# Performance work log

Hardware: AMD Instinct MI355X
Metric: run time of the kernel (lower is better)

Reference implementation:

```python
import jax, jax.numpy as jnp
import numpy as np

# levels for the auction iterations: j = 7..-1 gives level = -4^j, j = -2 gives level = 0
_LEVEL_JS = list(range(7, -3, -1))


def approx_match(xyz1, xyz2):
    # xyz1: [B,N,3], xyz2: [B,M,3] -> soft match matrix [B,N,M]
    B, N, _ = xyz1.shape
    M = xyz2.shape[1]
    multiL = 1.0 if N >= M else float(M // N)
    multiR = float(N // M) if N >= M else 1.0
    # pairwise squared distances [B,N,M]
    d2 = jnp.sum((xyz1[:, :, None, :] - xyz2[:, None, :, :]) ** 2, axis=-1)
    levels = jnp.array([0.0 if j == -2 else -(4.0 ** j) for j in _LEVEL_JS],
                       dtype=xyz1.dtype)

    def step(carry, level):
        match, remainL, remainR = carry
        w = jnp.exp(level * d2) * remainR[:, None, :]                      # [B,N,M]
        # row-normalize to each left point's remaining mass
        w = w * (remainL / (jnp.sum(w, axis=2) + 1e-9))[:, :, None]
        # clip columns to right points' remaining capacity
        ss = jnp.sum(w, axis=1) + 1e-9                                     # [B,M]
        w = w * jnp.minimum(remainR / ss, 1.0)[:, None, :]
        match = match + w
        remainL = jnp.maximum(remainL - jnp.sum(w, axis=2), 0.0)
        remainR = jnp.maximum(remainR - jnp.sum(w, axis=1), 0.0)
        return (match, remainL, remainR), None

    init = (jnp.zeros_like(d2),
            jnp.full((B, N), multiL, dtype=d2.dtype),
            jnp.full((B, M), multiR, dtype=d2.dtype))
    (match, _, _), _ = jax.lax.scan(step, init, levels)
    return match


def match_cost(xyz1, xyz2, match):
    # cost[b] = sum_{k,l} match[b,k,l] * ||xyz1[b,k] - xyz2[b,l]||
    d = jnp.sqrt(jnp.sum((xyz1[:, :, None, :] - xyz2[:, None, :, :]) ** 2, axis=-1))
    return jnp.sum(match * d, axis=(1, 2))


def setup_inputs() -> dict:
    key = jax.random.key(0)
    k1, k2 = jax.random.split(key)
    B, N, M = 8, 2048, 2048
    input1 = jax.random.normal(k1, (B, N, 3), dtype=jnp.float32)
    input2 = jax.random.normal(k2, (B, M, 3), dtype=jnp.float32)
    return {"input1": input1, "input2": input2}


def reference(input1, input2):
    match = approx_match(input1, input2)
    return match_cost(input1, input2, match)
```

## Files before the change

kernel.cpp:

```cpp
#include <hip/hip_runtime.h>
#include <hip/hip_fp16.h>


#define BATCH 8
#define NPTS 2048
#define MPTS 2048
#define BLOCK 256
#define ROWS 16
#define LOG2E 1.44269504088896340736f

__device__ __forceinline__ float fast_exp2(float x) {
  return __builtin_amdgcn_exp2f(x);
}
__device__ __forceinline__ float fast_sqrt(float a) {
  return __builtin_amdgcn_sqrtf(a);
}
__device__ __forceinline__ float packh2(float c, float r) {
  __half2 h = __halves2half2(__float2half_rn(c), __float2half_rn(r));
  return __builtin_bit_cast(float, h);
}

__device__ __forceinline__ void load8(const float4* q, int r0, float k,
                                      float* x, float* y, float* z) {
  int b4 = (r0 >> 2) * 3;
  float4 q0 = q[b4], q1 = q[b4 + 1], q2 = q[b4 + 2];
  float4 q3 = q[b4 + 3], q4 = q[b4 + 4], q5 = q[b4 + 5];
  x[0] = k * q0.x; y[0] = k * q0.y; z[0] = k * q0.z;
  x[1] = k * q0.w; y[1] = k * q1.x; z[1] = k * q1.y;
  x[2] = k * q1.z; y[2] = k * q1.w; z[2] = k * q2.x;
  x[3] = k * q2.y; y[3] = k * q2.z; z[3] = k * q2.w;
  x[4] = k * q3.x; y[4] = k * q3.y; z[4] = k * q3.z;
  x[5] = k * q3.w; y[5] = k * q4.x; z[5] = k * q4.y;
  x[6] = k * q4.z; y[6] = k * q4.w; z[6] = k * q5.x;
  x[7] = k * q5.y; y[7] = k * q5.z; z[7] = k * q5.w;
}

__global__ __launch_bounds__(BLOCK, 4) void emd_A0_kernel(
    const float* __restrict__ xyz1, const float* __restrict__ xyz2,
    float* __restrict__ rowscale, float* __restrict__ out,
    float* __restrict__ t9, float* __restrict__ t1acc,
    float* __restrict__ t1zero, float k0) {
  __shared__ float4 sP[MPTS];
  __shared__ float sRed[ROWS * 4];
  __shared__ float sRs[ROWS];

  const int tid = threadIdx.x;
  const int bid = blockIdx.x;
  const int b = bid >> 7;
  const int t0 = (bid & 127) * ROWS;
  const bool desig = (bid & 127) == 0;
  if (bid == 0 && tid < BATCH) { out[tid] = 0.0f; t9[tid] = 0.0f; }

  const float4* q2 = (const float4*)(xyz2 + (size_t)b * MPTS * 3);
  float4* z4 = (float4*)(t1zero + (size_t)b * MPTS);
  for (int g = tid; g < MPTS / 4; g += BLOCK) {
    float4 a = q2[3 * g], bb = q2[3 * g + 1], c = q2[3 * g + 2];
    sP[4 * g + 0] = make_float4(k0 * a.x, k0 * a.y, k0 * a.z, 0.0f);
    sP[4 * g + 1] = make_float4(k0 * a.w, k0 * bb.x, k0 * bb.y, 0.0f);
    sP[4 * g + 2] = make_float4(k0 * bb.z, k0 * bb.w, k0 * c.x, 0.0f);
    sP[4 * g + 3] = make_float4(k0 * c.y, k0 * c.z, k0 * c.w, 0.0f);
    if (desig) z4[g] = make_float4(0.f, 0.f, 0.f, 0.f);
  }
  __syncthreads();

  const int wave = tid >> 6, lane = tid & 63;
  const int phase = lane >> 1, rg = lane & 1;
  const int r0 = t0 + rg * 8;
  float x1[8], y1[8], z1[8], acc[8];
  load8((const float4*)(xyz1 + (size_t)b * NPTS * 3), r0, k0, x1, y1, z1);
#pragma unroll
  for (int j = 0; j < 8; ++j) acc[j] = 0.0f;
  const int mb = wave * 512 + phase;
#pragma unroll 2
  for (int it = 0; it < 16; ++it) {
    float4 v = sP[mb + it * 32];
#pragma unroll
    for (int j = 0; j < 8; ++j) {
      float dx = x1[j] - v.x, dy = y1[j] - v.y, dz = z1[j] - v.z;
      float s = __builtin_fmaf(dx, dx, __builtin_fmaf(dy, dy, dz * dz));
      acc[j] += fast_exp2(-s);
    }
  }
#pragma unroll
  for (int j = 0; j < 8; ++j) {
    acc[j] += __shfl_xor(acc[j], 2, 64);
    acc[j] += __shfl_xor(acc[j], 4, 64);
    acc[j] += __shfl_xor(acc[j], 8, 64);
    acc[j] += __shfl_xor(acc[j], 16, 64);
    acc[j] += __shfl_xor(acc[j], 32, 64);
  }
  if (lane < 2) {
#pragma unroll
    for (int j = 0; j < 8; ++j) sRed[(rg * 8 + j) * 4 + wave] = acc[j];
  }
  __syncthreads();
  if (tid < ROWS) {
    float s = sRed[tid * 4] + sRed[tid * 4 + 1] + sRed[tid * 4 + 2] +
              sRed[tid * 4 + 3];
    float rs = 1.0f / (s + 1e-9f);
    rowscale[(size_t)b * NPTS + t0 + tid] = rs;
    sRs[tid] = rs;
  }
  __syncthreads();

  float rsn[8];
#pragma unroll
  for (int j = 0; j < 8; ++j) rsn[j] = sRs[rg * 8 + j];
  float* accb = t1acc + (size_t)b * MPTS;
#pragma unroll 2
  for (int it = 0; it < 16; ++it) {
    int idx = mb + it * 32;
    float4 v = sP[idx];
    float part = 0.0f;
#pragma unroll
    for (int j = 0; j < 8; ++j) {
      float dx = x1[j] - v.x, dy = y1[j] - v.y, dz = z1[j] - v.z;
      float s = __builtin_fmaf(dx, dx, __builtin_fmaf(dy, dy, dz * dz));
      part = __builtin_fmaf(fast_exp2(-s), rsn[j], part);
    }
    part += __shfl_xor(part, 1, 64);
    if (rg == 0) atomicAdd(accb + idx, part);
  }
}

template <bool FIRST, bool LAST>
__global__ __launch_bounds__(BLOCK, 4) void emd_CA_kernel(
    const float* __restrict__ xyz1, const float* __restrict__ xyz2,
    float* __restrict__ rowscale, float* __restrict__ remainL,
    const float* __restrict__ rrIn, float* __restrict__ rrOut,
    const float* __restrict__ t1In, float* __restrict__ t1Acc,
    float* __restrict__ t1Zero, float* __restrict__ out,
    float* __restrict__ t9, float kS, float invK) {
  __shared__ float4 sP[MPTS];
  __shared__ float sRedS[ROWS * 4];
  __shared__ float sRedC[ROWS * 4];
  __shared__ float sRedR[ROWS * 4];
  __shared__ float sCost[ROWS];
  __shared__ float sRs[ROWS];

  const int tid = threadIdx.x;
  const int bid = blockIdx.x;
  const int b = bid >> 7;
  const int t0 = (bid & 127) * ROWS;
  const bool desig = (bid & 127) == 0;

  const float4* q2 = (const float4*)(xyz2 + (size_t)b * MPTS * 3);
  const float4* rr4 = (const float4*)(rrIn + (size_t)b * MPTS);
  const float4* t14 = (const float4*)(t1In + (size_t)b * MPTS);
  float4* ro4 = (float4*)(rrOut + (size_t)b * MPTS);
  float4* z4 = LAST ? nullptr : (float4*)(t1Zero + (size_t)b * MPTS);
  for (int g = tid; g < MPTS / 4; g += BLOCK) {
    float4 a = q2[3 * g], bb = q2[3 * g + 1], c = q2[3 * g + 2];
    float4 t1v = t14[g];
    float4 rrv = FIRST ? make_float4(1.f, 1.f, 1.f, 1.f) : rr4[g];
    float cc[4], rn[4];
    float rrc[4] = {rrv.x, rrv.y, rrv.z, rrv.w};
    float t1c[4] = {t1v.x, t1v.y, t1v.z, t1v.w};
#pragma unroll
    for (int i = 0; i < 4; ++i) {
      float colsum = rrc[i] * t1c[i];
      float cs = fminf(rrc[i] / (colsum + 1e-9f), 1.0f);
      cc[i] = rrc[i] * cs;
      rn[i] = fmaxf(rrc[i] - colsum * cs, 0.0f);
    }
    sP[4 * g + 0] = make_float4(kS * a.x, kS * a.y, kS * a.z, packh2(cc[0], rn[0]));
    sP[4 * g + 1] = make_float4(kS * a.w, kS * bb.x, kS * bb.y, packh2(cc[1], rn[1]));
    sP[4 * g + 2] = make_float4(kS * bb.z, kS * bb.w, kS * c.x, packh2(cc[2], rn[2]));
    sP[4 * g + 3] = make_float4(kS * c.y, kS * c.z, kS * c.w, packh2(cc[3], rn[3]));
    if (desig) {
      ro4[g] = make_float4(rn[0], rn[1], rn[2], rn[3]);
      if (!LAST) z4[g] = make_float4(0.f, 0.f, 0.f, 0.f);
    }
  }
  __syncthreads();

  const int wave = tid >> 6, lane = tid & 63;
  const int phase = lane >> 2, rg = lane & 3;
  const int r0 = t0 + rg * 4;
  float x1[4], y1[4], z1[4];
  {
    const float4* q1 = (const float4*)(xyz1 + (size_t)b * NPTS * 3);
    int b4 = (r0 >> 2) * 3;
    float4 a = q1[b4], bb = q1[b4 + 1], c = q1[b4 + 2];
    x1[0] = kS * a.x;  y1[0] = kS * a.y;  z1[0] = kS * a.z;
    x1[1] = kS * a.w;  y1[1] = kS * bb.x; z1[1] = kS * bb.y;
    x1[2] = kS * bb.z; y1[2] = kS * bb.w; z1[2] = kS * c.x;
    x1[3] = kS * c.y;  y1[3] = kS * c.z;  z1[3] = kS * c.w;
  }
  float accS[4] = {0.f, 0.f, 0.f, 0.f};
  float accC[4] = {0.f, 0.f, 0.f, 0.f};
  float accR[4] = {0.f, 0.f, 0.f, 0.f};
  const int mb = wave * 512 + phase;
#pragma unroll 4
  for (int it = 0; it < 32; ++it) {
    float4 v = sP[mb + it * 16];
    __half2 h = __builtin_bit_cast(__half2, v.w);
    float cc = __low2float(h);
    float rr = __high2float(h);
#pragma unroll
    for (int j = 0; j < 4; ++j) {
      float dx = x1[j] - v.x, dy = y1[j] - v.y, dz = z1[j] - v.z;
      float s = __builtin_fmaf(dx, dx, __builtin_fmaf(dy, dy, dz * dz));
      float sq = fast_sqrt(s);
      float e1, e2;
      if (LAST) {
        e2 = 1.0f;
        e1 = fast_exp2(-s);
      } else {
        e2 = fast_exp2(-s);
        float e2s = e2 * e2;
        e1 = e2s * e2s;
      }
      float t = e1 * cc;
      accS[j] += t;
      accC[j] = __builtin_fmaf(t, sq, accC[j]);
      if (LAST) accR[j] += rr;
      else      accR[j] = __builtin_fmaf(e2, rr, accR[j]);
    }
  }
#pragma unroll
  for (int j = 0; j < 4; ++j) {
    accS[j] += __shfl_xor(accS[j], 4, 64);
    accS[j] += __shfl_xor(accS[j], 8, 64);
    accS[j] += __shfl_xor(accS[j], 16, 64);
    accS[j] += __shfl_xor(accS[j], 32, 64);
    accC[j] += __shfl_xor(accC[j], 4, 64);
    accC[j] += __shfl_xor(accC[j], 8, 64);
    accC[j] += __shfl_xor(accC[j], 16, 64);
    accC[j] += __shfl_xor(accC[j], 32, 64);
    accR[j] += __shfl_xor(accR[j], 4, 64);
    accR[j] += __shfl_xor(accR[j], 8, 64);
    accR[j] += __shfl_xor(accR[j], 16, 64);
    accR[j] += __shfl_xor(accR[j], 32, 64);
  }
  if (lane < 4) {
#pragma unroll
    for (int j = 0; j < 4; ++j) {
      sRedS[(rg * 4 + j) * 4 + wave] = accS[j];
      sRedC[(rg * 4 + j) * 4 + wave] = accC[j];
      sRedR[(rg * 4 + j) * 4 + wave] = accR[j];
    }
  }
  __syncthreads();
  if (tid < ROWS) {
    float S2 = sRedS[tid * 4] + sRedS[tid * 4 + 1] + sRedS[tid * 4 + 2] +
               sRedS[tid * 4 + 3];
    float C = sRedC[tid * 4] + sRedC[tid * 4 + 1] + sRedC[tid * 4 + 2] +
              sRedC[tid * 4 + 3];
    float R = sRedR[tid * 4] + sRedR[tid * 4 + 1] + sRedR[tid * 4 + 2] +
              sRedR[tid * 4 + 3];
    size_t idx = (size_t)b * NPTS + t0 + tid;
    float rs = rowscale[idx];
    float rl = FIRST ? 1.0f : remainL[idx];
    float rlN = fmaxf(rl - rs * S2, 0.0f);
    remainL[idx] = rlN;
    float rsN = rlN / (R + 1e-9f);
    rowscale[idx] = rsN;
    sCost[tid] = rs * C * invK;
    sRs[tid] = rsN;
  }
  __syncthreads();
  if (tid == 0) {
    float t = 0.0f;
#pragma unroll
    for (int i = 0; i < ROWS; ++i) t += sCost[i];
    atomicAdd(out + b, t);
    if (LAST) {
      float r = 0.0f;
#pragma unroll
      for (int i = 0; i < ROWS; ++i) r += sRs[i];
      atomicAdd(t9 + b, r);
    }
  }
  if (!LAST) {
    float rsn[4];
#pragma unroll
    for (int j = 0; j < 4; ++j) rsn[j] = sRs[rg * 4 + j];
    float* accb = t1Acc + (size_t)b * MPTS;
#pragma unroll 4
    for (int it = 0; it < 32; ++it) {
      int idx = mb + it * 16;
      float4 v = sP[idx];
      float part = 0.0f;
#pragma unroll
      for (int j = 0; j < 4; ++j) {
        float dx = x1[j] - v.x, dy = y1[j] - v.y, dz = z1[j] - v.z;
        float s = __builtin_fmaf(dx, dx, __builtin_fmaf(dy, dy, dz * dz));
        part = __builtin_fmaf(fast_exp2(-s), rsn[j], part);
      }
      part += __shfl_xor(part, 1, 64);
      part += __shfl_xor(part, 2, 64);
      if (rg == 0) atomicAdd(accb + idx, part);
    }
  }
}

__global__ __launch_bounds__(BLOCK, 4) void emd_C9_kernel(
    const float* __restrict__ xyz1, const float* __restrict__ xyz2,
    const float* __restrict__ rowscale, const float* __restrict__ remainR,
    const float* __restrict__ t9, float* __restrict__ out) {
  __shared__ float4 sP[MPTS];
  __shared__ float sRed[ROWS * 4];
  __shared__ float sCost[ROWS];

  const int tid = threadIdx.x;
  const int bid = blockIdx.x;
  const int b = bid >> 7;
  const int t0 = (bid & 127) * ROWS;
  const int wave = tid >> 6, lane = tid & 63;
  const float t1 = t9[b];

  const float4* q2 = (const float4*)(xyz2 + (size_t)b * MPTS * 3);
  const float4* rr4 = (const float4*)(remainR + (size_t)b * MPTS);
  for (int g = tid; g < MPTS / 4; g += BLOCK) {
    float4 a = q2[3 * g], bb = q2[3 * g + 1], c = q2[3 * g + 2];
    float4 rr = rr4[g];
    float w0 = rr.x * fminf(rr.x / (rr.x * t1 + 1e-9f), 1.0f);
    float w1 = rr.y * fminf(rr.y / (rr.y * t1 + 1e-9f), 1.0f);
    float w2 = rr.z * fminf(rr.z / (rr.z * t1 + 1e-9f), 1.0f);
    float w3 = rr.w * fminf(rr.w / (rr.w * t1 + 1e-9f), 1.0f);
    sP[4 * g + 0] = make_float4(a.x, a.y, a.z, w0);
    sP[4 * g + 1] = make_float4(a.w, bb.x, bb.y, w1);
    sP[4 * g + 2] = make_float4(bb.z, bb.w, c.x, w2);
    sP[4 * g + 3] = make_float4(c.y, c.z, c.w, w3);
  }
  __syncthreads();

  const int phase = lane >> 1, rg = lane & 1;
  const int r0 = t0 + rg * 8;
  float x1[8], y1[8], z1[8], acc[8];
  load8((const float4*)(xyz1 + (size_t)b * NPTS * 3), r0, 1.0f, x1, y1, z1);
#pragma unroll
  for (int j = 0; j < 8; ++j) acc[j] = 0.0f;
  const int mb = wave * 512 + phase;
#pragma unroll 2
  for (int it = 0; it < 16; ++it) {
    float4 v = sP[mb + it * 32];
#pragma unroll
    for (int j = 0; j < 8; ++j) {
      float dx = x1[j] - v.x, dy = y1[j] - v.y, dz = z1[j] - v.z;
      float d2 = __builtin_fmaf(dx, dx, __builtin_fmaf(dy, dy, dz * dz));
      acc[j] = __builtin_fmaf(fast_sqrt(d2), v.w, acc[j]);
    }
  }
#pragma unroll
  for (int j = 0; j < 8; ++j) {
    acc[j] += __shfl_xor(acc[j], 2, 64);
    acc[j] += __shfl_xor(acc[j], 4, 64);
    acc[j] += __shfl_xor(acc[j], 8, 64);
    acc[j] += __shfl_xor(acc[j], 16, 64);
    acc[j] += __shfl_xor(acc[j], 32, 64);
  }
  if (lane < 2) {
#pragma unroll
    for (int j = 0; j < 8; ++j) sRed[(rg * 8 + j) * 4 + wave] = acc[j];
  }
  __syncthreads();
  if (tid < ROWS) {
    float C = sRed[tid * 4] + sRed[tid * 4 + 1] + sRed[tid * 4 + 2] +
              sRed[tid * 4 + 3];
    sCost[tid] = rowscale[(size_t)b * NPTS + t0 + tid] * C;
  }
  __syncthreads();
  if (tid == 0) {
    float t = 0.0f;
#pragma unroll
    for (int i = 0; i < ROWS; ++i) t += sCost[i];
    atomicAdd(out + b, t);
  }
}

extern "C" void kernel_launch(void* const* d_in, const int* in_sizes, int n_in,
                              void* d_out, int out_size, void* d_ws, size_t ws_size,
                              hipStream_t stream) {
  const float* xyz1 = (const float*)d_in[0];
  const float* xyz2 = (const float*)d_in[1];
  float* out = (float*)d_out;
  float* ws = (float*)d_ws;

  const int BN = BATCH * NPTS, BM = BATCH * MPTS;
  float* remainL  = ws;
  float* rowscale = ws + BN;
  float* rrA      = ws + 2 * BN;
  float* rrB      = ws + 2 * BN + BM;
  float* t1b      = ws + 2 * BN + 2 * BM;
  float* t9       = ws + 2 * BN + 5 * BM;

  const float levels[9] = {-16384.f, -4096.f, -1024.f, -256.f, -64.f,
                           -16.f,    -4.f,    -1.f,    -0.25f};
  dim3 grid(BATCH * (NPTS / ROWS));

  hipMemsetAsync(t1b, 0, (size_t)BM * sizeof(float), stream);

  emd_A0_kernel<<<grid, BLOCK, 0, stream>>>(
      xyz1, xyz2, rowscale, out, t9, t1b , t1b + BM ,
      sqrtf(-levels[0] * LOG2E));

  for (int l = 0; l < 9; ++l) {
    float kB = sqrtf(-levels[l] * LOG2E);
    float kA = 0.5f * kB;
    float* cur = t1b + (size_t)(l % 3) * BM;
    float* nxt = t1b + (size_t)((l + 1) % 3) * BM;
    float* zer = t1b + (size_t)((l + 2) % 3) * BM;
    float* rin = (l % 2 == 0) ? rrA : rrB;
    float* rou = (l % 2 == 0) ? rrB : rrA;
    if (l == 0) {
      emd_CA_kernel<true, false><<<grid, BLOCK, 0, stream>>>(
          xyz1, xyz2, rowscale, remainL, rin, rou, cur, nxt, zer, out, t9,
          kA, 1.0f / kA);
    } else if (l < 8) {
      emd_CA_kernel<false, false><<<grid, BLOCK, 0, stream>>>(
          xyz1, xyz2, rowscale, remainL, rin, rou, cur, nxt, zer, out, t9,
          kA, 1.0f / kA);
    } else {
      emd_CA_kernel<false, true><<<grid, BLOCK, 0, stream>>>(
          xyz1, xyz2, rowscale, remainL, rin, rou, cur, nxt, zer, out, t9,
          kB, 1.0f / kB);
    }
  }
  emd_C9_kernel<<<grid, BLOCK, 0, stream>>>(xyz1, xyz2, rowscale, rrB, t9, out);
}
```

Measured before the change: 357.4 us.

## Halve rows per block and stage xyz2 through LDS in two chunks

```diff
diff --git a/kernel.cpp b/kernel.cpp
--- a/kernel.cpp
+++ b/kernel.cpp
@@ -6,7 +6,8 @@
 #define NPTS 2048
 #define MPTS 2048
 #define BLOCK 256
-#define ROWS 16
+#define ROWS 8
+#define CHUNK 1024
 #define LOG2E 1.44269504088896340736f
 
 __device__ __forceinline__ float fast_exp2(float x) {
@@ -35,63 +36,77 @@
   x[7] = k * q5.y; y[7] = k * q5.z; z[7] = k * q5.w;
 }
 
-__global__ __launch_bounds__(BLOCK, 4) void emd_A0_kernel(
+__device__ __forceinline__ void load4(const float4* q, int r0, float k,
+                                      float* x, float* y, float* z) {
+  int b4 = (r0 >> 2) * 3;
+  float4 a = q[b4], bb = q[b4 + 1], c = q[b4 + 2];
+  x[0] = k * a.x;  y[0] = k * a.y;  z[0] = k * a.z;
+  x[1] = k * a.w;  y[1] = k * bb.x; z[1] = k * bb.y;
+  x[2] = k * bb.z; y[2] = k * bb.w; z[2] = k * c.x;
+  x[3] = k * c.y;  y[3] = k * c.z;  z[3] = k * c.w;
+}
+
+__global__ __launch_bounds__(BLOCK, 6) void emd_A0_kernel(
     const float* __restrict__ xyz1, const float* __restrict__ xyz2,
     float* __restrict__ rowscale, float* __restrict__ out,
     float* __restrict__ t9, float* __restrict__ t1acc,
     float* __restrict__ t1zero, float k0) {
-  __shared__ float4 sP[MPTS];
+  __shared__ float4 sP[CHUNK];
   __shared__ float sRed[ROWS * 4];
   __shared__ float sRs[ROWS];
 
   const int tid = threadIdx.x;
   const int bid = blockIdx.x;
-  const int b = bid >> 7;
-  const int t0 = (bid & 127) * ROWS;
-  const bool desig = (bid & 127) == 0;
+  const int b = bid >> 8;
+  const int t0 = (bid & 255) * ROWS;
+  const bool desig = (bid & 255) == 0;
   if (bid == 0 && tid < BATCH) { out[tid] = 0.0f; t9[tid] = 0.0f; }
 
+  const int wave = tid >> 6, lane = tid & 63;
   const float4* q2 = (const float4*)(xyz2 + (size_t)b * MPTS * 3);
   float4* z4 = (float4*)(t1zero + (size_t)b * MPTS);
-  for (int g = tid; g < MPTS / 4; g += BLOCK) {
-    float4 a = q2[3 * g], bb = q2[3 * g + 1], c = q2[3 * g + 2];
-    sP[4 * g + 0] = make_float4(k0 * a.x, k0 * a.y, k0 * a.z, 0.0f);
-    sP[4 * g + 1] = make_float4(k0 * a.w, k0 * bb.x, k0 * bb.y, 0.0f);
-    sP[4 * g + 2] = make_float4(k0 * bb.z, k0 * bb.w, k0 * c.x, 0.0f);
-    sP[4 * g + 3] = make_float4(k0 * c.y, k0 * c.z, k0 * c.w, 0.0f);
-    if (desig) z4[g] = make_float4(0.f, 0.f, 0.f, 0.f);
-  }
-  __syncthreads();
-
-  const int wave = tid >> 6, lane = tid & 63;
-  const int phase = lane >> 1, rg = lane & 1;
-  const int r0 = t0 + rg * 8;
+
   float x1[8], y1[8], z1[8], acc[8];
-  load8((const float4*)(xyz1 + (size_t)b * NPTS * 3), r0, k0, x1, y1, z1);
+  load8((const float4*)(xyz1 + (size_t)b * NPTS * 3), t0, k0, x1, y1, z1);
 #pragma unroll
   for (int j = 0; j < 8; ++j) acc[j] = 0.0f;
-  const int mb = wave * 512 + phase;
-#pragma unroll 2
-  for (int it = 0; it < 16; ++it) {
-    float4 v = sP[mb + it * 32];
-#pragma unroll
-    for (int j = 0; j < 8; ++j) {
-      float dx = x1[j] - v.x, dy = y1[j] - v.y, dz = z1[j] - v.z;
-      float s = __builtin_fmaf(dx, dx, __builtin_fmaf(dy, dy, dz * dz));
-      acc[j] += fast_exp2(-s);
+
+  for (int ch = 0; ch < 2; ++ch) {
+    __syncthreads();
+    {
+      const float4* qc = q2 + ch * (CHUNK * 3 / 4);
+      int g = tid;
+      float4 a = qc[3 * g], bb = qc[3 * g + 1], c = qc[3 * g + 2];
+      sP[4 * g + 0] = make_float4(k0 * a.x, k0 * a.y, k0 * a.z, 0.0f);
+      sP[4 * g + 1] = make_float4(k0 * a.w, k0 * bb.x, k0 * bb.y, 0.0f);
+      sP[4 * g + 2] = make_float4(k0 * bb.z, k0 * bb.w, k0 * c.x, 0.0f);
+      sP[4 * g + 3] = make_float4(k0 * c.y, k0 * c.z, k0 * c.w, 0.0f);
+      if (desig) z4[ch * 256 + g] = make_float4(0.f, 0.f, 0.f, 0.f);
+    }
+    __syncthreads();
+#pragma unroll
+    for (int it = 0; it < 4; ++it) {
+      float4 v = sP[wave * 256 + lane + it * 64];
+#pragma unroll
+      for (int j = 0; j < 8; ++j) {
+        float dx = x1[j] - v.x, dy = y1[j] - v.y, dz = z1[j] - v.z;
+        float s = __builtin_fmaf(dx, dx, __builtin_fmaf(dy, dy, dz * dz));
+        acc[j] += fast_exp2(-s);
+      }
     }
   }
 #pragma unroll
   for (int j = 0; j < 8; ++j) {
+    acc[j] += __shfl_xor(acc[j], 1, 64);
     acc[j] += __shfl_xor(acc[j], 2, 64);
     acc[j] += __shfl_xor(acc[j], 4, 64);
     acc[j] += __shfl_xor(acc[j], 8, 64);
     acc[j] += __shfl_xor(acc[j], 16, 64);
     acc[j] += __shfl_xor(acc[j], 32, 64);
   }
-  if (lane < 2) {
-#pragma unroll
-    for (int j = 0; j < 8; ++j) sRed[(rg * 8 + j) * 4 + wave] = acc[j];
+  if (lane == 0) {
+#pragma unroll
+    for (int j = 0; j < 8; ++j) sRed[j * 4 + wave] = acc[j];
   }
   __syncthreads();
   if (tid < ROWS) {
@@ -105,33 +120,45 @@
 
   float rsn[8];
 #pragma unroll
-  for (int j = 0; j < 8; ++j) rsn[j] = sRs[rg * 8 + j];
+  for (int j = 0; j < 8; ++j) rsn[j] = sRs[j];
   float* accb = t1acc + (size_t)b * MPTS;
-#pragma unroll 2
-  for (int it = 0; it < 16; ++it) {
-    int idx = mb + it * 32;
-    float4 v = sP[idx];
-    float part = 0.0f;
-#pragma unroll
-    for (int j = 0; j < 8; ++j) {
-      float dx = x1[j] - v.x, dy = y1[j] - v.y, dz = z1[j] - v.z;
-      float s = __builtin_fmaf(dx, dx, __builtin_fmaf(dy, dy, dz * dz));
-      part = __builtin_fmaf(fast_exp2(-s), rsn[j], part);
-    }
-    part += __shfl_xor(part, 1, 64);
-    if (rg == 0) atomicAdd(accb + idx, part);
+  for (int ch = 0; ch < 2; ++ch) {
+    __syncthreads();
+    {
+      const float4* qc = q2 + ch * (CHUNK * 3 / 4);
+      int g = tid;
+      float4 a = qc[3 * g], bb = qc[3 * g + 1], c = qc[3 * g + 2];
+      sP[4 * g + 0] = make_float4(k0 * a.x, k0 * a.y, k0 * a.z, 0.0f);
+      sP[4 * g + 1] = make_float4(k0 * a.w, k0 * bb.x, k0 * bb.y, 0.0f);
+      sP[4 * g + 2] = make_float4(k0 * bb.z, k0 * bb.w, k0 * c.x, 0.0f);
+      sP[4 * g + 3] = make_float4(k0 * c.y, k0 * c.z, k0 * c.w, 0.0f);
+    }
+    __syncthreads();
+#pragma unroll
+    for (int it = 0; it < 4; ++it) {
+      int idx = wave * 256 + lane + it * 64;
+      float4 v = sP[idx];
+      float part = 0.0f;
+#pragma unroll
+      for (int j = 0; j < 8; ++j) {
+        float dx = x1[j] - v.x, dy = y1[j] - v.y, dz = z1[j] - v.z;
+        float s = __builtin_fmaf(dx, dx, __builtin_fmaf(dy, dy, dz * dz));
+        part = __builtin_fmaf(fast_exp2(-s), rsn[j], part);
+      }
+      atomicAdd(accb + ch * CHUNK + idx, part);
+    }
   }
 }
 
 template <bool FIRST, bool LAST>
-__global__ __launch_bounds__(BLOCK, 4) void emd_CA_kernel(
+__global__ __launch_bounds__(BLOCK, 6) void emd_CA_kernel(
     const float* __restrict__ xyz1, const float* __restrict__ xyz2,
     float* __restrict__ rowscale, float* __restrict__ remainL,
     const float* __restrict__ rrIn, float* __restrict__ rrOut,
     const float* __restrict__ t1In, float* __restrict__ t1Acc,
     float* __restrict__ t1Zero, float* __restrict__ out,
     float* __restrict__ t9, float kS, float invK) {
-  __shared__ float4 sP[MPTS];
+  __shared__ float4 sP[CHUNK];
   __shared__ float sRedS[ROWS * 4];
   __shared__ float sRedC[ROWS * 4];
   __shared__ float sRedR[ROWS * 4];
@@ -140,100 +167,100 @@
 
   const int tid = threadIdx.x;
   const int bid = blockIdx.x;
-  const int b = bid >> 7;
-  const int t0 = (bid & 127) * ROWS;
-  const bool desig = (bid & 127) == 0;
+  const int b = bid >> 8;
+  const int t0 = (bid & 255) * ROWS;
+  const bool desig = (bid & 255) == 0;
+  const int wave = tid >> 6, lane = tid & 63;
+  const int rg = lane & 1, phase = lane >> 1;
+  const int r0 = t0 + rg * 4;
 
   const float4* q2 = (const float4*)(xyz2 + (size_t)b * MPTS * 3);
   const float4* rr4 = (const float4*)(rrIn + (size_t)b * MPTS);
   const float4* t14 = (const float4*)(t1In + (size_t)b * MPTS);
   float4* ro4 = (float4*)(rrOut + (size_t)b * MPTS);
   float4* z4 = LAST ? nullptr : (float4*)(t1Zero + (size_t)b * MPTS);
-  for (int g = tid; g < MPTS / 4; g += BLOCK) {
-    float4 a = q2[3 * g], bb = q2[3 * g + 1], c = q2[3 * g + 2];
-    float4 t1v = t14[g];
-    float4 rrv = FIRST ? make_float4(1.f, 1.f, 1.f, 1.f) : rr4[g];
-    float cc[4], rn[4];
-    float rrc[4] = {rrv.x, rrv.y, rrv.z, rrv.w};
-    float t1c[4] = {t1v.x, t1v.y, t1v.z, t1v.w};
-#pragma unroll
-    for (int i = 0; i < 4; ++i) {
-      float colsum = rrc[i] * t1c[i];
-      float cs = fminf(rrc[i] / (colsum + 1e-9f), 1.0f);
-      cc[i] = rrc[i] * cs;
-      rn[i] = fmaxf(rrc[i] - colsum * cs, 0.0f);
-    }
-    sP[4 * g + 0] = make_float4(kS * a.x, kS * a.y, kS * a.z, packh2(cc[0], rn[0]));
-    sP[4 * g + 1] = make_float4(kS * a.w, kS * bb.x, kS * bb.y, packh2(cc[1], rn[1]));
-    sP[4 * g + 2] = make_float4(kS * bb.z, kS * bb.w, kS * c.x, packh2(cc[2], rn[2]));
-    sP[4 * g + 3] = make_float4(kS * c.y, kS * c.z, kS * c.w, packh2(cc[3], rn[3]));
-    if (desig) {
-      ro4[g] = make_float4(rn[0], rn[1], rn[2], rn[3]);
-      if (!LAST) z4[g] = make_float4(0.f, 0.f, 0.f, 0.f);
-    }
-  }
-  __syncthreads();
-
-  const int wave = tid >> 6, lane = tid & 63;
-  const int phase = lane >> 2, rg = lane & 3;
-  const int r0 = t0 + rg * 4;
+
   float x1[4], y1[4], z1[4];
-  {
-    const float4* q1 = (const float4*)(xyz1 + (size_t)b * NPTS * 3);
-    int b4 = (r0 >> 2) * 3;
-    float4 a = q1[b4], bb = q1[b4 + 1], c = q1[b4 + 2];
-    x1[0] = kS * a.x;  y1[0] = kS * a.y;  z1[0] = kS * a.z;
-    x1[1] = kS * a.w;  y1[1] = kS * bb.x; z1[1] = kS * bb.y;
-    x1[2] = kS * bb.z; y1[2] = kS * bb.w; z1[2] = kS * c.x;
-    x1[3] = kS * c.y;  y1[3] = kS * c.z;  z1[3] = kS * c.w;
-  }
+  load4((const float4*)(xyz1 + (size_t)b * NPTS * 3), r0, kS, x1, y1, z1);
   float accS[4] = {0.f, 0.f, 0.f, 0.f};
   float accC[4] = {0.f, 0.f, 0.f, 0.f};
   float accR[4] = {0.f, 0.f, 0.f, 0.f};
-  const int mb = wave * 512 + phase;
-#pragma unroll 4
-  for (int it = 0; it < 32; ++it) {
-    float4 v = sP[mb + it * 16];
-    __half2 h = __builtin_bit_cast(__half2, v.w);
-    float cc = __low2float(h);
-    float rr = __high2float(h);
-#pragma unroll
-    for (int j = 0; j < 4; ++j) {
-      float dx = x1[j] - v.x, dy = y1[j] - v.y, dz = z1[j] - v.z;
-      float s = __builtin_fmaf(dx, dx, __builtin_fmaf(dy, dy, dz * dz));
-      float sq = fast_sqrt(s);
-      float e1, e2;
-      if (LAST) {
-        e2 = 1.0f;
-        e1 = fast_exp2(-s);
-      } else {
-        e2 = fast_exp2(-s);
-        float e2s = e2 * e2;
-        e1 = e2s * e2s;
-      }
-      float t = e1 * cc;
-      accS[j] += t;
-      accC[j] = __builtin_fmaf(t, sq, accC[j]);
-      if (LAST) accR[j] += rr;
-      else      accR[j] = __builtin_fmaf(e2, rr, accR[j]);
+
+  for (int ch = 0; ch < 2; ++ch) {
+    __syncthreads();
+    {
+      const float4* qc = q2 + ch * (CHUNK * 3 / 4);
+      int g = tid;
+      float4 a = qc[3 * g], bb = qc[3 * g + 1], c = qc[3 * g + 2];
+      float4 t1v = t14[ch * 256 + g];
+      float4 rrv = FIRST ? make_float4(1.f, 1.f, 1.f, 1.f) : rr4[ch * 256 + g];
+      float cc[4], rn[4];
+      float rrc[4] = {rrv.x, rrv.y, rrv.z, rrv.w};
+      float t1c[4] = {t1v.x, t1v.y, t1v.z, t1v.w};
+#pragma unroll
+      for (int i = 0; i < 4; ++i) {
+        float colsum = rrc[i] * t1c[i];
+        float cs = fminf(rrc[i] / (colsum + 1e-9f), 1.0f);
+        cc[i] = rrc[i] * cs;
+        rn[i] = fmaxf(rrc[i] - colsum * cs, 0.0f);
+      }
+      sP[4 * g + 0] = make_float4(kS * a.x, kS * a.y, kS * a.z, packh2(cc[0], rn[0]));
+      sP[4 * g + 1] = make_float4(kS * a.w, kS * bb.x, kS * bb.y, packh2(cc[1], rn[1]));
+      sP[4 * g + 2] = make_float4(kS * bb.z, kS * bb.w, kS * c.x, packh2(cc[2], rn[2]));
+      sP[4 * g + 3] = make_float4(kS * c.y, kS * c.z, kS * c.w, packh2(cc[3], rn[3]));
+      if (desig) {
+        ro4[ch * 256 + g] = make_float4(rn[0], rn[1], rn[2], rn[3]);
+        if (!LAST) z4[ch * 256 + g] = make_float4(0.f, 0.f, 0.f, 0.f);
+      }
+    }
+    __syncthreads();
+#pragma unroll
+    for (int it = 0; it < 8; ++it) {
+      float4 v = sP[wave * 256 + phase + it * 32];
+      __half2 h = __builtin_bit_cast(__half2, v.w);
+      float cc = __low2float(h);
+      float rr = __high2float(h);
+#pragma unroll
+      for (int j = 0; j < 4; ++j) {
+        float dx = x1[j] - v.x, dy = y1[j] - v.y, dz = z1[j] - v.z;
+        float s = __builtin_fmaf(dx, dx, __builtin_fmaf(dy, dy, dz * dz));
+        float sq = fast_sqrt(s);
+        float e1, e2;
+        if (LAST) {
+          e2 = 1.0f;
+          e1 = fast_exp2(-s);
+        } else {
+          e2 = fast_exp2(-s);
+          float e2s = e2 * e2;
+          e1 = e2s * e2s;
+        }
+        float t = e1 * cc;
+        accS[j] += t;
+        accC[j] = __builtin_fmaf(t, sq, accC[j]);
+        if (LAST) accR[j] += rr;
+        else      accR[j] = __builtin_fmaf(e2, rr, accR[j]);
+      }
     }
   }
 #pragma unroll
   for (int j = 0; j < 4; ++j) {
+    accS[j] += __shfl_xor(accS[j], 2, 64);
     accS[j] += __shfl_xor(accS[j], 4, 64);
     accS[j] += __shfl_xor(accS[j], 8, 64);
     accS[j] += __shfl_xor(accS[j], 16, 64);
     accS[j] += __shfl_xor(accS[j], 32, 64);
+    accC[j] += __shfl_xor(accC[j], 2, 64);
     accC[j] += __shfl_xor(accC[j], 4, 64);
     accC[j] += __shfl_xor(accC[j], 8, 64);
     accC[j] += __shfl_xor(accC[j], 16, 64);
     accC[j] += __shfl_xor(accC[j], 32, 64);
+    accR[j] += __shfl_xor(accR[j], 2, 64);
     accR[j] += __shfl_xor(accR[j], 4, 64);
     accR[j] += __shfl_xor(accR[j], 8, 64);
     accR[j] += __shfl_xor(accR[j], 16, 64);
     accR[j] += __shfl_xor(accR[j], 32, 64);
   }
-  if (lane < 4) {
+  if (lane < 2) {
 #pragma unroll
     for (int j = 0; j < 4; ++j) {
       sRedS[(rg * 4 + j) * 4 + wave] = accS[j];
@@ -277,83 +304,99 @@
 #pragma unroll
     for (int j = 0; j < 4; ++j) rsn[j] = sRs[rg * 4 + j];
     float* accb = t1Acc + (size_t)b * MPTS;
-#pragma unroll 4
-    for (int it = 0; it < 32; ++it) {
-      int idx = mb + it * 16;
-      float4 v = sP[idx];
-      float part = 0.0f;
-#pragma unroll
-      for (int j = 0; j < 4; ++j) {
-        float dx = x1[j] - v.x, dy = y1[j] - v.y, dz = z1[j] - v.z;
-        float s = __builtin_fmaf(dx, dx, __builtin_fmaf(dy, dy, dz * dz));
-        part = __builtin_fmaf(fast_exp2(-s), rsn[j], part);
-      }
-      part += __shfl_xor(part, 1, 64);
-      part += __shfl_xor(part, 2, 64);
-      if (rg == 0) atomicAdd(accb + idx, part);
-    }
-  }
-}
-
-__global__ __launch_bounds__(BLOCK, 4) void emd_C9_kernel(
+    for (int ch = 0; ch < 2; ++ch) {
+      __syncthreads();
+      {
+        const float4* qc = q2 + ch * (CHUNK * 3 / 4);
+        int g = tid;
+        float4 a = qc[3 * g], bb = qc[3 * g + 1], c = qc[3 * g + 2];
+        sP[4 * g + 0] = make_float4(kS * a.x, kS * a.y, kS * a.z, 0.0f);
+        sP[4 * g + 1] = make_float4(kS * a.w, kS * bb.x, kS * bb.y, 0.0f);
+        sP[4 * g + 2] = make_float4(kS * bb.z, kS * bb.w, kS * c.x, 0.0f);
+        sP[4 * g + 3] = make_float4(kS * c.y, kS * c.z, kS * c.w, 0.0f);
+      }
+      __syncthreads();
+#pragma unroll
+      for (int it = 0; it < 8; ++it) {
+        int idx = wave * 256 + phase + it * 32;
+        float4 v = sP[idx];
+        float part = 0.0f;
+#pragma unroll
+        for (int j = 0; j < 4; ++j) {
+          float dx = x1[j] - v.x, dy = y1[j] - v.y, dz = z1[j] - v.z;
+          float s = __builtin_fmaf(dx, dx, __builtin_fmaf(dy, dy, dz * dz));
+          part = __builtin_fmaf(fast_exp2(-s), rsn[j], part);
+        }
+        part += __shfl_xor(part, 1, 64);
+        if (rg == 0) atomicAdd(accb + ch * CHUNK + idx, part);
+      }
+    }
+  }
+}
+
+__global__ __launch_bounds__(BLOCK, 6) void emd_C9_kernel(
     const float* __restrict__ xyz1, const float* __restrict__ xyz2,
     const float* __restrict__ rowscale, const float* __restrict__ remainR,
     const float* __restrict__ t9, float* __restrict__ out) {
-  __shared__ float4 sP[MPTS];
+  __shared__ float4 sP[CHUNK];
   __shared__ float sRed[ROWS * 4];
   __shared__ float sCost[ROWS];
 
   const int tid = threadIdx.x;
   const int bid = blockIdx.x;
-  const int b = bid >> 7;
-  const int t0 = (bid & 127) * ROWS;
+  const int b = bid >> 8;
+  const int t0 = (bid & 255) * ROWS;
   const int wave = tid >> 6, lane = tid & 63;
   const float t1 = t9[b];
 
   const float4* q2 = (const float4*)(xyz2 + (size_t)b * MPTS * 3);
   const float4* rr4 = (const float4*)(remainR + (size_t)b * MPTS);
-  for (int g = tid; g < MPTS / 4; g += BLOCK) {
-    float4 a = q2[3 * g], bb = q2[3 * g + 1], c = q2[3 * g + 2];
-    float4 rr = rr4[g];
-    float w0 = rr.x * fminf(rr.x / (rr.x * t1 + 1e-9f), 1.0f);
-    float w1 = rr.y * fminf(rr.y / (rr.y * t1 + 1e-9f), 1.0f);
-    float w2 = rr.z * fminf(rr.z / (rr.z * t1 + 1e-9f), 1.0f);
-    float w3 = rr.w * fminf(rr.w / (rr.w * t1 + 1e-9f), 1.0f);
-    sP[4 * g + 0] = make_float4(a.x, a.y, a.z, w0);
-    sP[4 * g + 1] = make_float4(a.w, bb.x, bb.y, w1);
-    sP[4 * g + 2] = make_float4(bb.z, bb.w, c.x, w2);
-    sP[4 * g + 3] = make_float4(c.y, c.z, c.w, w3);
-  }
-  __syncthreads();
-
-  const int phase = lane >> 1, rg = lane & 1;
-  const int r0 = t0 + rg * 8;
+
   float x1[8], y1[8], z1[8], acc[8];
-  load8((const float4*)(xyz1 + (size_t)b * NPTS * 3), r0, 1.0f, x1, y1, z1);
+  load8((const float4*)(xyz1 + (size_t)b * NPTS * 3), t0, 1.0f, x1, y1, z1);
 #pragma unroll
   for (int j = 0; j < 8; ++j) acc[j] = 0.0f;
-  const int mb = wave * 512 + phase;
-#pragma unroll 2
-  for (int it = 0; it < 16; ++it) {
-    float4 v = sP[mb + it * 32];
-#pragma unroll
-    for (int j = 0; j < 8; ++j) {
-      float dx = x1[j] - v.x, dy = y1[j] - v.y, dz = z1[j] - v.z;
-      float d2 = __builtin_fmaf(dx, dx, __builtin_fmaf(dy, dy, dz * dz));
-      acc[j] = __builtin_fmaf(fast_sqrt(d2), v.w, acc[j]);
+
+  for (int ch = 0; ch < 2; ++ch) {
+    __syncthreads();
+    {
+      const float4* qc = q2 + ch * (CHUNK * 3 / 4);
+      int g = tid;
+      float4 a = qc[3 * g], bb = qc[3 * g + 1], c = qc[3 * g + 2];
+      float4 rr = rr4[ch * 256 + g];
+      float w0 = rr.x * fminf(rr.x / (rr.x * t1 + 1e-9f), 1.0f);
+      float w1 = rr.y * fminf(rr.y / (rr.y * t1 + 1e-9f), 1.0f);
+      float w2 = rr.z * fminf(rr.z / (rr.z * t1 + 1e-9f), 1.0f);
+      float w3 = rr.w * fminf(rr.w / (rr.w * t1 + 1e-9f), 1.0f);
+      sP[4 * g + 0] = make_float4(a.x, a.y, a.z, w0);
+      sP[4 * g + 1] = make_float4(a.w, bb.x, bb.y, w1);
+      sP[4 * g + 2] = make_float4(bb.z, bb.w, c.x, w2);
+      sP[4 * g + 3] = make_float4(c.y, c.z, c.w, w3);
+    }
+    __syncthreads();
+#pragma unroll
+    for (int it = 0; it < 4; ++it) {
+      float4 v = sP[wave * 256 + lane + it * 64];
+#pragma unroll
+      for (int j = 0; j < 8; ++j) {
+        float dx = x1[j] - v.x, dy = y1[j] - v.y, dz = z1[j] - v.z;
+        float d2 = __builtin_fmaf(dx, dx, __builtin_fmaf(dy, dy, dz * dz));
+        acc[j] = __builtin_fmaf(fast_sqrt(d2), v.w, acc[j]);
+      }
     }
   }
 #pragma unroll
   for (int j = 0; j < 8; ++j) {
+    acc[j] += __shfl_xor(acc[j], 1, 64);
     acc[j] += __shfl_xor(acc[j], 2, 64);
     acc[j] += __shfl_xor(acc[j], 4, 64);
     acc[j] += __shfl_xor(acc[j], 8, 64);
     acc[j] += __shfl_xor(acc[j], 16, 64);
     acc[j] += __shfl_xor(acc[j], 32, 64);
   }
-  if (lane < 2) {
-#pragma unroll
-    for (int j = 0; j < 8; ++j) sRed[(rg * 8 + j) * 4 + wave] = acc[j];
+  if (lane == 0) {
+#pragma unroll
+    for (int j = 0; j < 8; ++j) sRed[j * 4 + wave] = acc[j];
   }
   __syncthreads();
   if (tid < ROWS) {
@@ -393,7 +436,7 @@
   hipMemsetAsync(t1b, 0, (size_t)BM * sizeof(float), stream);
 
   emd_A0_kernel<<<grid, BLOCK, 0, stream>>>(
-      xyz1, xyz2, rowscale, out, t9, t1b , t1b + BM ,
+      xyz1, xyz2, rowscale, out, t9, t1b, t1b + BM,
       sqrtf(-levels[0] * LOG2E));
 
   for (int l = 0; l < 9; ++l) {
```

Result: slower. 1.131 ms (+216.4%).

## Replace global column-sum atomics with per-block partials and a reduction kernel

Applied to the files above, without the earlier changes.

```diff
diff --git a/kernel.cpp b/kernel.cpp
--- a/kernel.cpp
+++ b/kernel.cpp
@@ -7,6 +7,7 @@
 #define MPTS 2048
 #define BLOCK 256
 #define ROWS 16
+#define KBLK 128
 #define LOG2E 1.44269504088896340736f
 
 __device__ __forceinline__ float fast_exp2(float x) {
@@ -38,8 +39,7 @@
 __global__ __launch_bounds__(BLOCK, 4) void emd_A0_kernel(
     const float* __restrict__ xyz1, const float* __restrict__ xyz2,
     float* __restrict__ rowscale, float* __restrict__ out,
-    float* __restrict__ t9, float* __restrict__ t1acc,
-    float* __restrict__ t1zero, float k0) {
+    float* __restrict__ t9, float* __restrict__ partials, float k0) {
   __shared__ float4 sP[MPTS];
   __shared__ float sRed[ROWS * 4];
   __shared__ float sRs[ROWS];
@@ -47,19 +47,17 @@
   const int tid = threadIdx.x;
   const int bid = blockIdx.x;
   const int b = bid >> 7;
-  const int t0 = (bid & 127) * ROWS;
-  const bool desig = (bid & 127) == 0;
+  const int blk = bid & 127;
+  const int t0 = blk * ROWS;
   if (bid == 0 && tid < BATCH) { out[tid] = 0.0f; t9[tid] = 0.0f; }
 
   const float4* q2 = (const float4*)(xyz2 + (size_t)b * MPTS * 3);
-  float4* z4 = (float4*)(t1zero + (size_t)b * MPTS);
   for (int g = tid; g < MPTS / 4; g += BLOCK) {
     float4 a = q2[3 * g], bb = q2[3 * g + 1], c = q2[3 * g + 2];
     sP[4 * g + 0] = make_float4(k0 * a.x, k0 * a.y, k0 * a.z, 0.0f);
     sP[4 * g + 1] = make_float4(k0 * a.w, k0 * bb.x, k0 * bb.y, 0.0f);
     sP[4 * g + 2] = make_float4(k0 * bb.z, k0 * bb.w, k0 * c.x, 0.0f);
     sP[4 * g + 3] = make_float4(k0 * c.y, k0 * c.z, k0 * c.w, 0.0f);
-    if (desig) z4[g] = make_float4(0.f, 0.f, 0.f, 0.f);
   }
   __syncthreads();
 
@@ -106,7 +104,7 @@
   float rsn[8];
 #pragma unroll
   for (int j = 0; j < 8; ++j) rsn[j] = sRs[rg * 8 + j];
-  float* accb = t1acc + (size_t)b * MPTS;
+  float* pb = partials + ((size_t)b * KBLK + blk) * MPTS;
 #pragma unroll 2
   for (int it = 0; it < 16; ++it) {
     int idx = mb + it * 32;
@@ -119,8 +117,25 @@
       part = __builtin_fmaf(fast_exp2(-s), rsn[j], part);
     }
     part += __shfl_xor(part, 1, 64);
-    if (rg == 0) atomicAdd(accb + idx, part);
-  }
+    if (rg == 0) pb[idx] = part;
+  }
+}
+
+__global__ __launch_bounds__(BLOCK) void emd_red_kernel(
+    const float* __restrict__ partials, float* __restrict__ t1) {
+  const int tid = threadIdx.x, bid = blockIdx.x;
+  const int b = bid >> 3;
+  const int m = (bid & 7) * BLOCK + tid;
+  const float* p = partials + (size_t)b * KBLK * MPTS + m;
+  float s0 = 0.f, s1 = 0.f, s2 = 0.f, s3 = 0.f;
+#pragma unroll 4
+  for (int k = 0; k < KBLK; k += 4) {
+    s0 += p[(size_t)(k + 0) * MPTS];
+    s1 += p[(size_t)(k + 1) * MPTS];
+    s2 += p[(size_t)(k + 2) * MPTS];
+    s3 += p[(size_t)(k + 3) * MPTS];
+  }
+  t1[(size_t)b * MPTS + m] = (s0 + s1) + (s2 + s3);
 }
 
 template <bool FIRST, bool LAST>
@@ -128,9 +143,8 @@
     const float* __restrict__ xyz1, const float* __restrict__ xyz2,
     float* __restrict__ rowscale, float* __restrict__ remainL,
     const float* __restrict__ rrIn, float* __restrict__ rrOut,
-    const float* __restrict__ t1In, float* __restrict__ t1Acc,
-    float* __restrict__ t1Zero, float* __restrict__ out,
-    float* __restrict__ t9, float kS, float invK) {
+    const float* __restrict__ t1In, float* __restrict__ partials,
+    float* __restrict__ out, float* __restrict__ t9, float kS, float invK) {
   __shared__ float4 sP[MPTS];
   __shared__ float sRedS[ROWS * 4];
   __shared__ float sRedC[ROWS * 4];
@@ -141,14 +155,14 @@
   const int tid = threadIdx.x;
   const int bid = blockIdx.x;
   const int b = bid >> 7;
-  const int t0 = (bid & 127) * ROWS;
-  const bool desig = (bid & 127) == 0;
+  const int blk = bid & 127;
+  const int t0 = blk * ROWS;
+  const bool desig = blk == 0;
 
   const float4* q2 = (const float4*)(xyz2 + (size_t)b * MPTS * 3);
   const float4* rr4 = (const float4*)(rrIn + (size_t)b * MPTS);
   const float4* t14 = (const float4*)(t1In + (size_t)b * MPTS);
   float4* ro4 = (float4*)(rrOut + (size_t)b * MPTS);
-  float4* z4 = LAST ? nullptr : (float4*)(t1Zero + (size_t)b * MPTS);
   for (int g = tid; g < MPTS / 4; g += BLOCK) {
     float4 a = q2[3 * g], bb = q2[3 * g + 1], c = q2[3 * g + 2];
     float4 t1v = t14[g];
@@ -167,10 +181,7 @@
     sP[4 * g + 1] = make_float4(kS * a.w, kS * bb.x, kS * bb.y, packh2(cc[1], rn[1]));
     sP[4 * g + 2] = make_float4(kS * bb.z, kS * bb.w, kS * c.x, packh2(cc[2], rn[2]));
     sP[4 * g + 3] = make_float4(kS * c.y, kS * c.z, kS * c.w, packh2(cc[3], rn[3]));
-    if (desig) {
-      ro4[g] = make_float4(rn[0], rn[1], rn[2], rn[3]);
-      if (!LAST) z4[g] = make_float4(0.f, 0.f, 0.f, 0.f);
-    }
+    if (desig) ro4[g] = make_float4(rn[0], rn[1], rn[2], rn[3]);
   }
   __syncthreads();
 
@@ -276,7 +287,7 @@
     float rsn[4];
 #pragma unroll
     for (int j = 0; j < 4; ++j) rsn[j] = sRs[rg * 4 + j];
-    float* accb = t1Acc + (size_t)b * MPTS;
+    float* pb = partials + ((size_t)b * KBLK + blk) * MPTS;
 #pragma unroll 4
     for (int it = 0; it < 32; ++it) {
       int idx = mb + it * 16;
@@ -290,7 +301,7 @@
       }
       part += __shfl_xor(part, 1, 64);
       part += __shfl_xor(part, 2, 64);
-      if (rg == 0) atomicAdd(accb + idx, part);
+      if (rg == 0) pb[idx] = part;
     }
   }
 }
@@ -383,40 +394,39 @@
   float* rowscale = ws + BN;
   float* rrA      = ws + 2 * BN;
   float* rrB      = ws + 2 * BN + BM;
-  float* t1b      = ws + 2 * BN + 2 * BM;
-  float* t9       = ws + 2 * BN + 5 * BM;
+  float* t1       = ws + 2 * BN + 2 * BM;
+  float* t9       = ws + 2 * BN + 3 * BM;
+  float* partials = ws + 2 * BN + 3 * BM + 16;
 
   const float levels[9] = {-16384.f, -4096.f, -1024.f, -256.f, -64.f,
                            -16.f,    -4.f,    -1.f,    -0.25f};
   dim3 grid(BATCH * (NPTS / ROWS));
-
-  hipMemsetAsync(t1b, 0, (size_t)BM * sizeof(float), stream);
+  dim3 rgrid(BATCH * (MPTS / BLOCK));
 
   emd_A0_kernel<<<grid, BLOCK, 0, stream>>>(
-      xyz1, xyz2, rowscale, out, t9, t1b , t1b + BM ,
-      sqrtf(-levels[0] * LOG2E));
+      xyz1, xyz2, rowscale, out, t9, partials, sqrtf(-levels[0] * LOG2E));
+  emd_red_kernel<<<rgrid, BLOCK, 0, stream>>>(partials, t1);
 
   for (int l = 0; l < 9; ++l) {
     float kB = sqrtf(-levels[l] * LOG2E);
     float kA = 0.5f * kB;
-    float* cur = t1b + (size_t)(l % 3) * BM;
-    float* nxt = t1b + (size_t)((l + 1) % 3) * BM;
-    float* zer = t1b + (size_t)((l + 2) % 3) * BM;
     float* rin = (l % 2 == 0) ? rrA : rrB;
     float* rou = (l % 2 == 0) ? rrB : rrA;
     if (l == 0) {
       emd_CA_kernel<true, false><<<grid, BLOCK, 0, stream>>>(
-          xyz1, xyz2, rowscale, remainL, rin, rou, cur, nxt, zer, out, t9,
+          xyz1, xyz2, rowscale, remainL, rin, rou, t1, partials, out, t9,
           kA, 1.0f / kA);
     } else if (l < 8) {
       emd_CA_kernel<false, false><<<grid, BLOCK, 0, stream>>>(
-          xyz1, xyz2, rowscale, remainL, rin, rou, cur, nxt, zer, out, t9,
+          xyz1, xyz2, rowscale, remainL, rin, rou, t1, partials, out, t9,
           kA, 1.0f / kA);
     } else {
       emd_CA_kernel<false, true><<<grid, BLOCK, 0, stream>>>(
-          xyz1, xyz2, rowscale, remainL, rin, rou, cur, nxt, zer, out, t9,
+          xyz1, xyz2, rowscale, remainL, rin, rou, t1, partials, out, t9,
           kB, 1.0f / kB);
     }
+    if (l < 8)
+      emd_red_kernel<<<rgrid, BLOCK, 0, stream>>>(partials, t1);
   }
   emd_C9_kernel<<<grid, BLOCK, 0, stream>>>(xyz1, xyz2, rowscale, rrB, t9, out);
 }
```

Result: slower. 468.9 us (+31.2%).
